# Kernel tuning notes

Measured on AMD Instinct MI355X. Metric: run time of the kernel, lower is better.

## Reference

```python
import jax, jax.numpy as jnp
import numpy as np

B, N, C, H = 2, 4096, 384, 6
HD = C // H          # 64
HALF = C // 2        # 192 = 3 pose heads * HD
MLP_H = 4 * C        # 1536
EPS = 1e-5


def _ln(x, g, b):
    m = jnp.mean(x, axis=-1, keepdims=True)
    v = jnp.mean((x - m) ** 2, axis=-1, keepdims=True)
    return (x - m) * jax.lax.rsqrt(v + EPS) * g + b


def setup_inputs() -> dict:
    key = jax.random.key(0)
    ks = jax.random.split(key, 6)
    s = 0.02
    return {
        "x": jax.random.normal(ks[0], (B, N, C), dtype=jnp.float32),
        "qkv_w": jax.random.normal(ks[1], (3 * C, C), dtype=jnp.float32) * s,
        "proj_w": jax.random.normal(ks[2], (C, HALF), dtype=jnp.float32) * s,
        "proj_b": jnp.zeros((C,), jnp.float32),
        "gamma1": jnp.ones((C,), jnp.float32),
        "beta1": jnp.zeros((C,), jnp.float32),
        "gamma2": jnp.ones((C,), jnp.float32),
        "beta2": jnp.zeros((C,), jnp.float32),
        "fc1_w": jax.random.normal(ks[3], (MLP_H, C), dtype=jnp.float32) * s,
        "fc1_b": jnp.zeros((MLP_H,), jnp.float32),
        "fc2_w": jax.random.normal(ks[4], (C, MLP_H), dtype=jnp.float32) * s,
        "fc2_b": jnp.zeros((C,), jnp.float32),
    }


def reference(x, qkv_w, proj_w, proj_b, gamma1, beta1, gamma2, beta2,
              fc1_w, fc1_b, fc2_w, fc2_b):
    b, n, c = x.shape
    scale = HD ** -0.5
    # --- attention on pre-norm input ---
    h = _ln(x, gamma1, beta1)
    qkv = (h @ qkv_w.T).reshape(b, n, 3, H, HD).transpose(2, 0, 3, 1, 4)  # [3,B,H,N,HD]
    q, k, v = qkv[0], qkv[1], qkv[2]
    # obj heads 0:3 -> sigmoid attention; pose heads 3:6 -> softmax attention
    attn_obj = jax.nn.sigmoid(jnp.einsum('bhnd,bhmd->bhnm', q[:, :3], k[:, :3]) * scale)
    attn_pose = jax.nn.softmax(jnp.einsum('bhnd,bhmd->bhnm', q[:, 3:], k[:, 3:]) * scale, axis=-1)
    # chained combine: pose-attn applied after obj-attn on pose values
    ctx = jnp.einsum('bhnm,bhmd->bhnd', attn_obj, v[:, 3:])      # [B,3,N,HD]
    ctx = jnp.einsum('bhnm,bhmd->bhnd', attn_pose, ctx)          # [B,3,N,HD]
    ctx = ctx.transpose(0, 2, 1, 3).reshape(b, n, HALF)          # [B,N,C/2]
    x = x + (ctx @ proj_w.T + proj_b)
    # --- MLP ---
    h2 = _ln(x, gamma2, beta2)
    mlp = jax.nn.gelu(h2 @ fc1_w.T + fc1_b, approximate=False) @ fc2_w.T + fc2_b
    return (x + mlp, attn_obj)
```

## Files before the change

### kernel.cpp

```cpp
#include <hip/hip_runtime.h>
#include <hip/hip_bf16.h>
#include <cmath>


typedef __hip_bfloat16 bf16;
typedef __attribute__((ext_vector_type(8))) short short8;
typedef __attribute__((ext_vector_type(4))) short s16x4;
typedef __attribute__((ext_vector_type(4))) float f32x4;

#define MFMA16(a, b, c) __builtin_amdgcn_mfma_f32_16x16x32_bf16((a), (b), (c), 0, 0, 0)

__device__ __forceinline__ void async16(const void* g, void* l) {
  __builtin_amdgcn_global_load_lds(
      (const __attribute__((address_space(1))) void*)g,
      (__attribute__((address_space(3))) void*)l, 16, 0, 0);
}

__device__ __forceinline__ short f2bs(float v) {
  union { bf16 b; short s; } u;
  u.b = __float2bfloat16(v);
  return u.s;
}

__global__ void cvt_f32_bf16(const float* __restrict__ in, bf16* __restrict__ out, int n) {
  int i = blockIdx.x * 256 + threadIdx.x;
  if (i < n) out[i] = __float2bfloat16(in[i]);
}

__global__ __launch_bounds__(128) void ln_fwd(const float* __restrict__ x,
                                              const float* __restrict__ gamma,
                                              const float* __restrict__ beta,
                                              bf16* __restrict__ out) {
  const int row = blockIdx.x;
  const int t = threadIdx.x;
  const float* xr = x + (size_t)row * 384;
  float v0 = xr[t], v1 = xr[t + 128], v2 = xr[t + 256];
  float s = v0 + v1 + v2;
  float q = v0 * v0 + v1 * v1 + v2 * v2;
#pragma unroll
  for (int m = 1; m < 64; m <<= 1) {
    s += __shfl_xor(s, m);
    q += __shfl_xor(q, m);
  }
  __shared__ float ss[2], qq[2];
  int w = t >> 6;
  if ((t & 63) == 0) { ss[w] = s; qq[w] = q; }
  __syncthreads();
  s = ss[0] + ss[1];
  q = qq[0] + qq[1];
  float mean = s * (1.0f / 384.0f);
  float var = q * (1.0f / 384.0f) - mean * mean;
  float rstd = rsqrtf(var + 1e-5f);
  bf16* orow = out + (size_t)row * 384;
  orow[t]       = __float2bfloat16((v0 - mean) * rstd * gamma[t]       + beta[t]);
  orow[t + 128] = __float2bfloat16((v1 - mean) * rstd * gamma[t + 128] + beta[t + 128]);
  orow[t + 256] = __float2bfloat16((v2 - mean) * rstd * gamma[t + 256] + beta[t + 256]);
}

template <int EPI>
__global__ __launch_bounds__(256) void gemm_nt(const bf16* __restrict__ A,
                                               const bf16* __restrict__ Bm, int M, int N, int K,
                                               const float* __restrict__ bias,
                                               const float* __restrict__ resid,
                                               float* __restrict__ outf,
                                               bf16* __restrict__ outb) {
  __shared__ __attribute__((aligned(16))) short As[2][64][64];
  __shared__ __attribute__((aligned(16))) short Bs[2][128][64];
  const int t = threadIdx.x;
  const int l = t & 63;
  const int w = t >> 6;
  const int bm = blockIdx.y * 64, bn = blockIdx.x * 128;
  const int r8 = t >> 3, c8 = (t & 7) * 8;

  const bf16* Ab = A + (size_t)(bm + r8) * K + c8;
  const bf16* Bb = Bm + (size_t)(bn + r8) * K + c8;

  f32x4 acc[4][2] = {};

  auto stage = [&](int kt, int bf) {
    async16(Ab + kt, &As[bf][r8][c8]);
    async16(Ab + (size_t)32 * K + kt, &As[bf][32 + r8][c8]);
#pragma unroll
    for (int i = 0; i < 4; ++i)
      async16(Bb + (size_t)(i * 32) * K + kt, &Bs[bf][i * 32 + r8][c8]);
  };

  stage(0, 0);
  int bf = 0;
  for (int kt = 0; kt < K; kt += 64) {
    __syncthreads();
    if (kt + 64 < K) stage(kt + 64, bf ^ 1);
#pragma unroll
    for (int ks = 0; ks < 2; ++ks) {
      short8 a[4], b[2];
#pragma unroll
      for (int i = 0; i < 4; ++i)
        a[i] = *(const short8*)&As[bf][i * 16 + (l & 15)][ks * 32 + (l >> 4) * 8];
#pragma unroll
      for (int j = 0; j < 2; ++j)
        b[j] = *(const short8*)&Bs[bf][w * 32 + j * 16 + (l & 15)][ks * 32 + (l >> 4) * 8];
#pragma unroll
      for (int i = 0; i < 4; ++i)
#pragma unroll
        for (int j = 0; j < 2; ++j) acc[i][j] = MFMA16(a[i], b[j], acc[i][j]);
    }
    bf ^= 1;
  }

#pragma unroll
  for (int i = 0; i < 4; ++i) {
#pragma unroll
    for (int j = 0; j < 2; ++j) {
#pragma unroll
      for (int r = 0; r < 4; ++r) {
        int row = bm + i * 16 + (l >> 4) * 4 + r;
        int col = bn + w * 32 + j * 16 + (l & 15);
        float v = acc[i][j][r];
        if (EPI == 0) {
          int three = col / 384;
          int rem = col - three * 384;
          int head = rem >> 6;
          int hd = rem & 63;
          int bb = row >> 12;
          int n = row & 4095;
          const size_t QSZ = (size_t)2 * 6 * 4096 * 64;
          if (three < 2) {
            size_t di = ((((size_t)three * 2 + bb) * 6 + head) * 4096 + n) * 64 + hd;
            outb[di] = __float2bfloat16(v);
          } else {
            size_t di = 2 * QSZ + (((size_t)bb * 6 + head) * 64 + hd) * 4096 + n;
            outb[di] = __float2bfloat16(v);
          }
        } else if (EPI == 1 || EPI == 3) {
          size_t di = (size_t)row * N + col;
          outf[di] = v + bias[col] + resid[di];
        } else if (EPI == 2) {
          float u = v + bias[col];
          float z = 0.7978845608f * (u + 0.044715f * u * u * u);
          float e = __builtin_amdgcn_exp2f(z * 2.885390082f);
          float th = 1.0f - 2.0f * __builtin_amdgcn_rcpf(e + 1.0f);
          outb[(size_t)row * N + col] = __float2bfloat16(0.5f * u * (1.0f + th));
        }
      }
    }
  }
}

template <int MODE>
__global__ __launch_bounds__(256) void attn_fused(const bf16* __restrict__ qkvb,
                                                  const bf16* __restrict__ vsrc_base,
                                                  float* __restrict__ aout,
                                                  float* __restrict__ part,
                                                  float* __restrict__ lpart) {
  const int bh = blockIdx.z, b = bh / 3, h = bh - b * 3;
  const int row0 = blockIdx.x * 64;
  const int cbase = blockIdx.y * 1024;
  const int t = threadIdx.x, l = t & 63, w = t >> 6;

  const size_t HSZ = (size_t)4096 * 64;
  const size_t QSZ = (size_t)2 * 6 * 4096 * 64;
  const int head = (MODE == 0) ? h : h + 3;
  const bf16* qp = qkvb + (size_t)(b * 6 + head) * HSZ;
  const bf16* kp = qkvb + QSZ + (size_t)(b * 6 + head) * HSZ;
  const bf16* vbase = (MODE == 0)
      ? qkvb + 2 * QSZ + (size_t)((b * 6 + h + 3) * 64) * 4096
      : vsrc_base + (size_t)(bh * 64) * 4096;

  __shared__ __attribute__((aligned(16))) short Ks[2][64][64];
  __shared__ __attribute__((aligned(16))) short Vs[2][64][64];
  __shared__ __attribute__((aligned(16))) float Sf[4][16][68];

  short8 aq[2];
  {
    int qrow = row0 + w * 16 + (l & 15);
    const bf16* qq = qp + (size_t)qrow * 64 + (l >> 4) * 8;
    aq[0] = *(const short8*)(qq);
    aq[1] = *(const short8*)(qq + 32);
  }

  const int r8 = t >> 3, c8 = (t & 7) * 8;
  const int sc = c8 ^ ((r8 & 7) * 8);

  auto stage = [&](int ct, int bf) {
    const bf16* kb = kp + (size_t)(cbase + ct * 64) * 64;
    async16(kb + (size_t)r8 * 64 + sc, &Ks[bf][r8][c8]);
    async16(kb + (size_t)(32 + r8) * 64 + sc, &Ks[bf][32 + r8][c8]);
    const bf16* vb = vbase + cbase + ct * 64;
    async16(vb + (size_t)r8 * 4096 + sc, &Vs[bf][r8][c8]);
    async16(vb + (size_t)(32 + r8) * 4096 + sc, &Vs[bf][32 + r8][c8]);
  };

  f32x4 cacc[4] = {};
  float lp[4] = {0.f, 0.f, 0.f, 0.f};
  const float K1 = -0.18033688f;
  const float K2 = 0.18033688f;

  float* sfw = &Sf[w][0][0];
  stage(0, 0);
  int bf = 0;
  for (int ct = 0; ct < 16; ++ct) {
    __syncthreads();
    if (ct < 15) stage(ct + 1, bf ^ 1);

    f32x4 sacc[4] = {};
#pragma unroll
    for (int ks = 0; ks < 2; ++ks) {
#pragma unroll
      for (int j = 0; j < 4; ++j) {
        int rr = j * 16 + (l & 15);
        int ec = (ks * 32 + (l >> 4) * 8) ^ ((rr & 7) * 8);
        short8 bk = *(const short8*)&Ks[bf][rr][ec];
        sacc[j] = MFMA16(aq[ks], bk, sacc[j]);
      }
    }

#pragma unroll
    for (int j = 0; j < 4; ++j) {
#pragma unroll
      for (int r = 0; r < 4; ++r) {
        float s = sacc[j][r];
        float v;
        if (MODE == 0) {
          v = __builtin_amdgcn_rcpf(1.0f + __builtin_amdgcn_exp2f(s * K1));
        } else {
          v = __builtin_amdgcn_exp2f(s * K2);
          lp[r] += v;
        }
        sfw[((l >> 4) * 4 + r) * 68 + j * 16 + (l & 15)] = v;
      }
    }

    short8 pa[2];
#pragma unroll
    for (int ks = 0; ks < 2; ++ks) {
      const float* sp = &sfw[(l & 15) * 68 + ks * 32 + (l >> 4) * 8];
      f32x4 f0 = *(const f32x4*)sp;
      f32x4 f1 = *(const f32x4*)(sp + 4);
      short8 a;
#pragma unroll
      for (int e = 0; e < 4; ++e) a[e] = f2bs(f0[e]);
#pragma unroll
      for (int e = 0; e < 4; ++e) a[4 + e] = f2bs(f1[e]);
      pa[ks] = a;
    }

    if (MODE == 0) {
      float* ab = aout + (size_t)bh * 4096 * 4096 +
                  (size_t)(row0 + w * 16) * 4096 + cbase + ct * 64;
#pragma unroll
      for (int i = 0; i < 4; ++i) {
        f32x4 vv = *(const f32x4*)&sfw[(4 * i + (l >> 4)) * 68 + (l & 15) * 4];
        *(f32x4*)(ab + (size_t)(4 * i + (l >> 4)) * 4096 + (l & 15) * 4) = vv;
      }
    }

#pragma unroll
    for (int ks = 0; ks < 2; ++ks) {
#pragma unroll
      for (int j = 0; j < 4; ++j) {
        int rr = j * 16 + (l & 15);
        int ec = (ks * 32 + (l >> 4) * 8) ^ ((rr & 7) * 8);
        short8 bv = *(const short8*)&Vs[bf][rr][ec];
        cacc[j] = MFMA16(pa[ks], bv, cacc[j]);
      }
    }
    bf ^= 1;
  }

  float* pb = part + ((size_t)(blockIdx.y * 6 + bh) * 4096 + row0 + w * 16) * 64;
#pragma unroll
  for (int j = 0; j < 4; ++j)
#pragma unroll
    for (int r = 0; r < 4; ++r)
      pb[(size_t)((l >> 4) * 4 + r) * 64 + j * 16 + (l & 15)] = cacc[j][r];

  if (MODE == 1) {
#pragma unroll
    for (int r = 0; r < 4; ++r) {
#pragma unroll
      for (int m = 1; m < 16; m <<= 1) lp[r] += __shfl_xor(lp[r], m);
    }
    if ((l & 15) == 0) {
      float* lb = lpart + (size_t)(blockIdx.y * 6 + bh) * 4096 + row0 + w * 16 + (l >> 4) * 4;
#pragma unroll
      for (int r = 0; r < 4; ++r) lb[r] = lp[r];
    }
  }
}

__global__ __launch_bounds__(256) void reduce_obj(const float* __restrict__ part,
                                                  bf16* __restrict__ ctx1T) {
  const int bh = blockIdx.y, n0 = blockIdx.x * 64, t = threadIdx.x;
  __shared__ short S[64][66];
  const int nr = t >> 2, h0 = (t & 3) * 16;
  const size_t CS = (size_t)6 * 4096 * 64;
  const float* p0 = part + ((size_t)bh * 4096 + n0 + nr) * 64 + h0;
#pragma unroll
  for (int q = 0; q < 4; ++q) {
    f32x4 s = {};
#pragma unroll
    for (int c = 0; c < 4; ++c) s += *(const f32x4*)(p0 + c * CS + q * 4);
#pragma unroll
    for (int e = 0; e < 4; ++e) S[nr][h0 + q * 4 + e] = f2bs(s[e]);
  }
  __syncthreads();
  const int hd = t >> 2, nb = (t & 3) * 16;
  short8 o0, o1;
#pragma unroll
  for (int k = 0; k < 8; ++k) o0[k] = S[nb + k][hd];
#pragma unroll
  for (int k = 0; k < 8; ++k) o1[k] = S[nb + 8 + k][hd];
  short* dst = (short*)(ctx1T + ((size_t)bh * 64 + hd) * 4096 + n0 + nb);
  *(short8*)dst = o0;
  *(short8*)(dst + 8) = o1;
}

__global__ __launch_bounds__(256) void reduce_pose(const float* __restrict__ part,
                                                   const float* __restrict__ lpart,
                                                   bf16* __restrict__ ctxf) {
  const int idx = blockIdx.x * 256 + threadIdx.x;
  const int hd4 = idx & 15;
  const int n = (idx >> 4) & 4095;
  const int bh = idx >> 16;
  const size_t CS = (size_t)6 * 4096 * 64, CL = (size_t)6 * 4096;
  f32x4 s = {};
  float lt = 0.f;
#pragma unroll
  for (int c = 0; c < 4; ++c) {
    s += *(const f32x4*)(part + c * CS + ((size_t)bh * 4096 + n) * 64 + hd4 * 4);
    lt += lpart[c * CL + (size_t)bh * 4096 + n];
  }
  float inv = 1.0f / lt;
  int b = bh / 3, h = bh - b * 3;
  s16x4 o;
#pragma unroll
  for (int e = 0; e < 4; ++e) o[e] = f2bs(s[e] * inv);
  *(s16x4*)(ctxf + ((size_t)b * 4096 + n) * 192 + h * 64 + hd4 * 4) = o;
}

extern "C" void kernel_launch(void* const* d_in, const int* in_sizes, int n_in,
                              void* d_out, int out_size, void* d_ws, size_t ws_size,
                              hipStream_t stream) {
  const float* x      = (const float*)d_in[0];
  const float* qkv_w  = (const float*)d_in[1];
  const float* proj_w = (const float*)d_in[2];
  const float* proj_b = (const float*)d_in[3];
  const float* gamma1 = (const float*)d_in[4];
  const float* beta1  = (const float*)d_in[5];
  const float* gamma2 = (const float*)d_in[6];
  const float* beta2  = (const float*)d_in[7];
  const float* fc1_w  = (const float*)d_in[8];
  const float* fc1_b  = (const float*)d_in[9];
  const float* fc2_w  = (const float*)d_in[10];
  const float* fc2_b  = (const float*)d_in[11];

  float* out_x = (float*)d_out;
  float* out_attn = out_x + (size_t)2 * 4096 * 384;

  char* ws = (char*)d_ws;
  size_t off = 0;
  auto alloc = [&](size_t bytes) -> void* {
    void* p = ws + off;
    off += (bytes + 255) & ~(size_t)255;
    return p;
  };
  bf16* qkv_w_b  = (bf16*)alloc((size_t)1152 * 384 * 2);
  bf16* proj_w_b = (bf16*)alloc((size_t)384 * 192 * 2);
  bf16* fc1_w_b  = (bf16*)alloc((size_t)1536 * 384 * 2);
  bf16* fc2_w_b  = (bf16*)alloc((size_t)384 * 1536 * 2);
  bf16* h1    = (bf16*)alloc((size_t)8192 * 384 * 2);
  bf16* qkvb  = (bf16*)alloc((size_t)3 * 2 * 6 * 4096 * 64 * 2);
  float* c1p  = (float*)alloc((size_t)4 * 6 * 4096 * 64 * 4);
  float* cpp  = (float*)alloc((size_t)4 * 6 * 4096 * 64 * 4);
  float* lpp  = (float*)alloc((size_t)4 * 6 * 4096 * 4);
  bf16* ctx1T = (bf16*)alloc((size_t)6 * 64 * 4096 * 2);
  bf16* ctxf  = (bf16*)alloc((size_t)2 * 4096 * 192 * 2);
  float* x2   = (float*)alloc((size_t)8192 * 384 * 4);
  bf16* h2    = (bf16*)alloc((size_t)8192 * 384 * 2);
  bf16* h3    = (bf16*)alloc((size_t)8192 * 1536 * 2);

  cvt_f32_bf16<<<(1152 * 384 + 255) / 256, 256, 0, stream>>>(qkv_w, qkv_w_b, 1152 * 384);
  cvt_f32_bf16<<<(384 * 192 + 255) / 256, 256, 0, stream>>>(proj_w, proj_w_b, 384 * 192);
  cvt_f32_bf16<<<(1536 * 384 + 255) / 256, 256, 0, stream>>>(fc1_w, fc1_w_b, 1536 * 384);
  cvt_f32_bf16<<<(384 * 1536 + 255) / 256, 256, 0, stream>>>(fc2_w, fc2_w_b, 384 * 1536);

  ln_fwd<<<8192, 128, 0, stream>>>(x, gamma1, beta1, h1);

  gemm_nt<0><<<dim3(9, 128), 256, 0, stream>>>(h1, qkv_w_b, 8192, 1152, 384,
                                               nullptr, nullptr, nullptr, qkvb);

  attn_fused<0><<<dim3(64, 4, 6), 256, 0, stream>>>(qkvb, nullptr, out_attn, c1p, nullptr);
  reduce_obj<<<dim3(64, 6), 256, 0, stream>>>(c1p, ctx1T);
  attn_fused<1><<<dim3(64, 4, 6), 256, 0, stream>>>(qkvb, ctx1T, nullptr, cpp, lpp);
  reduce_pose<<<1536, 256, 0, stream>>>(cpp, lpp, ctxf);

  gemm_nt<1><<<dim3(3, 128), 256, 0, stream>>>(ctxf, proj_w_b, 8192, 384, 192,
                                               proj_b, x, x2, nullptr);
  ln_fwd<<<8192, 128, 0, stream>>>(x2, gamma2, beta2, h2);
  gemm_nt<2><<<dim3(12, 128), 256, 0, stream>>>(h2, fc1_w_b, 8192, 1536, 384,
                                                fc1_b, nullptr, nullptr, h3);
  gemm_nt<3><<<dim3(3, 128), 256, 0, stream>>>(h3, fc2_w_b, 8192, 384, 1536,
                                               fc2_b, x2, out_x, nullptr);
}
```

Before: 310.8 us.

## Enlarge GEMM and attention tiles, merge weight casts, one-wave-per-row LayerNorm

Attention blocks now process 128 query rows instead of 64, so each staged K/V tile is reused across two row fragments and half as many blocks reload K/V. The QKV and fc1 GEMMs move to a 128x128 tile with a 2x2 wave layout but lose double buffering, since staging is now synchronous with two barriers per K step. The four weight-cast launches become one kernel, and LayerNorm uses one wave per row with no shared-memory reduction. The single-buffered GEMM exposes global-load latency, and the larger attention tile adds register pressure and halves the grid.

```diff
diff --git a/kernel.cpp b/kernel.cpp
--- a/kernel.cpp
+++ b/kernel.cpp
@@ -22,99 +22,102 @@
   return u.s;
 }
 
-__global__ void cvt_f32_bf16(const float* __restrict__ in, bf16* __restrict__ out, int n) {
+__global__ void cvt_all(const float* __restrict__ a, const float* __restrict__ b,
+                        const float* __restrict__ c, const float* __restrict__ d,
+                        bf16* __restrict__ oa, bf16* __restrict__ ob,
+                        bf16* __restrict__ oc, bf16* __restrict__ od) {
   int i = blockIdx.x * 256 + threadIdx.x;
-  if (i < n) out[i] = __float2bfloat16(in[i]);
-}
-
-__global__ __launch_bounds__(128) void ln_fwd(const float* __restrict__ x,
+  const int n0 = 1152 * 384, n1 = 384 * 192, n2 = 1536 * 384, n3 = 384 * 1536;
+  if (i < n0) { oa[i] = __float2bfloat16(a[i]); return; }
+  i -= n0;
+  if (i < n1) { ob[i] = __float2bfloat16(b[i]); return; }
+  i -= n1;
+  if (i < n2) { oc[i] = __float2bfloat16(c[i]); return; }
+  i -= n2;
+  if (i < n3) { od[i] = __float2bfloat16(d[i]); }
+}
+
+__global__ __launch_bounds__(256) void ln_fwd(const float* __restrict__ x,
                                               const float* __restrict__ gamma,
                                               const float* __restrict__ beta,
                                               bf16* __restrict__ out) {
-  const int row = blockIdx.x;
-  const int t = threadIdx.x;
+  const int row = blockIdx.x * 4 + (threadIdx.x >> 6);
+  const int l = threadIdx.x & 63;
   const float* xr = x + (size_t)row * 384;
-  float v0 = xr[t], v1 = xr[t + 128], v2 = xr[t + 256];
-  float s = v0 + v1 + v2;
-  float q = v0 * v0 + v1 * v1 + v2 * v2;
+  float v[6];
+  float s = 0.f, q = 0.f;
+#pragma unroll
+  for (int i = 0; i < 6; ++i) {
+    v[i] = xr[l + i * 64];
+    s += v[i];
+    q += v[i] * v[i];
+  }
 #pragma unroll
   for (int m = 1; m < 64; m <<= 1) {
     s += __shfl_xor(s, m);
     q += __shfl_xor(q, m);
   }
-  __shared__ float ss[2], qq[2];
-  int w = t >> 6;
-  if ((t & 63) == 0) { ss[w] = s; qq[w] = q; }
-  __syncthreads();
-  s = ss[0] + ss[1];
-  q = qq[0] + qq[1];
   float mean = s * (1.0f / 384.0f);
   float var = q * (1.0f / 384.0f) - mean * mean;
   float rstd = rsqrtf(var + 1e-5f);
   bf16* orow = out + (size_t)row * 384;
-  orow[t]       = __float2bfloat16((v0 - mean) * rstd * gamma[t]       + beta[t]);
-  orow[t + 128] = __float2bfloat16((v1 - mean) * rstd * gamma[t + 128] + beta[t + 128]);
-  orow[t + 256] = __float2bfloat16((v2 - mean) * rstd * gamma[t + 256] + beta[t + 256]);
+#pragma unroll
+  for (int i = 0; i < 6; ++i)
+    orow[l + i * 64] = __float2bfloat16((v[i] - mean) * rstd * gamma[l + i * 64] + beta[l + i * 64]);
 }
 
 template <int EPI>
-__global__ __launch_bounds__(256) void gemm_nt(const bf16* __restrict__ A,
+__global__ __launch_bounds__(256) void gemm128(const bf16* __restrict__ A,
                                                const bf16* __restrict__ Bm, int M, int N, int K,
                                                const float* __restrict__ bias,
-                                               const float* __restrict__ resid,
-                                               float* __restrict__ outf,
                                                bf16* __restrict__ outb) {
-  __shared__ __attribute__((aligned(16))) short As[2][64][64];
-  __shared__ __attribute__((aligned(16))) short Bs[2][128][64];
+  __shared__ __attribute__((aligned(16))) short As[128][64];
+  __shared__ __attribute__((aligned(16))) short Bs[128][64];
   const int t = threadIdx.x;
   const int l = t & 63;
   const int w = t >> 6;
-  const int bm = blockIdx.y * 64, bn = blockIdx.x * 128;
-  const int r8 = t >> 3, c8 = (t & 7) * 8;
-
+  const int wm = w >> 1, wn = w & 1;
+  const int bm = blockIdx.y * 128, bn = blockIdx.x * 128;
+
+  f32x4 acc[4][4] = {};
+  const int r8 = t >> 3;
+  const int c8 = (t & 7) * 8;
   const bf16* Ab = A + (size_t)(bm + r8) * K + c8;
   const bf16* Bb = Bm + (size_t)(bn + r8) * K + c8;
 
-  f32x4 acc[4][2] = {};
-
-  auto stage = [&](int kt, int bf) {
-    async16(Ab + kt, &As[bf][r8][c8]);
-    async16(Ab + (size_t)32 * K + kt, &As[bf][32 + r8][c8]);
-#pragma unroll
-    for (int i = 0; i < 4; ++i)
-      async16(Bb + (size_t)(i * 32) * K + kt, &Bs[bf][i * 32 + r8][c8]);
-  };
-
-  stage(0, 0);
-  int bf = 0;
   for (int kt = 0; kt < K; kt += 64) {
     __syncthreads();
-    if (kt + 64 < K) stage(kt + 64, bf ^ 1);
+#pragma unroll
+    for (int i = 0; i < 4; ++i)
+      async16(Ab + (size_t)(i * 32) * K + kt, &As[i * 32 + r8][c8]);
+#pragma unroll
+    for (int i = 0; i < 4; ++i)
+      async16(Bb + (size_t)(i * 32) * K + kt, &Bs[i * 32 + r8][c8]);
+    __syncthreads();
 #pragma unroll
     for (int ks = 0; ks < 2; ++ks) {
-      short8 a[4], b[2];
+      short8 a[4], b[4];
 #pragma unroll
       for (int i = 0; i < 4; ++i)
-        a[i] = *(const short8*)&As[bf][i * 16 + (l & 15)][ks * 32 + (l >> 4) * 8];
-#pragma unroll
-      for (int j = 0; j < 2; ++j)
-        b[j] = *(const short8*)&Bs[bf][w * 32 + j * 16 + (l & 15)][ks * 32 + (l >> 4) * 8];
+        a[i] = *(const short8*)&As[wm * 64 + i * 16 + (l & 15)][ks * 32 + (l >> 4) * 8];
 #pragma unroll
       for (int i = 0; i < 4; ++i)
-#pragma unroll
-        for (int j = 0; j < 2; ++j) acc[i][j] = MFMA16(a[i], b[j], acc[i][j]);
-    }
-    bf ^= 1;
+        b[i] = *(const short8*)&Bs[wn * 64 + i * 16 + (l & 15)][ks * 32 + (l >> 4) * 8];
+#pragma unroll
+      for (int i = 0; i < 4; ++i)
+#pragma unroll
+        for (int j = 0; j < 4; ++j) acc[i][j] = MFMA16(a[i], b[j], acc[i][j]);
+    }
   }
 
 #pragma unroll
   for (int i = 0; i < 4; ++i) {
 #pragma unroll
-    for (int j = 0; j < 2; ++j) {
+    for (int j = 0; j < 4; ++j) {
 #pragma unroll
       for (int r = 0; r < 4; ++r) {
-        int row = bm + i * 16 + (l >> 4) * 4 + r;
-        int col = bn + w * 32 + j * 16 + (l & 15);
+        int row = bm + wm * 64 + i * 16 + (l >> 4) * 4 + r;
+        int col = bn + wn * 64 + j * 16 + (l & 15);
         float v = acc[i][j][r];
         if (EPI == 0) {
           int three = col / 384;
@@ -131,16 +134,76 @@
             size_t di = 2 * QSZ + (((size_t)bb * 6 + head) * 64 + hd) * 4096 + n;
             outb[di] = __float2bfloat16(v);
           }
-        } else if (EPI == 1 || EPI == 3) {
-          size_t di = (size_t)row * N + col;
-          outf[di] = v + bias[col] + resid[di];
-        } else if (EPI == 2) {
+        } else {
           float u = v + bias[col];
           float z = 0.7978845608f * (u + 0.044715f * u * u * u);
           float e = __builtin_amdgcn_exp2f(z * 2.885390082f);
           float th = 1.0f - 2.0f * __builtin_amdgcn_rcpf(e + 1.0f);
           outb[(size_t)row * N + col] = __float2bfloat16(0.5f * u * (1.0f + th));
         }
+      }
+    }
+  }
+}
+
+__global__ __launch_bounds__(256) void gemm64(const bf16* __restrict__ A,
+                                              const bf16* __restrict__ Bm, int M, int N, int K,
+                                              const float* __restrict__ bias,
+                                              const float* __restrict__ resid,
+                                              float* __restrict__ outf) {
+  __shared__ __attribute__((aligned(16))) short As[2][64][64];
+  __shared__ __attribute__((aligned(16))) short Bs[2][128][64];
+  const int t = threadIdx.x;
+  const int l = t & 63;
+  const int w = t >> 6;
+  const int bm = blockIdx.y * 64, bn = blockIdx.x * 128;
+  const int r8 = t >> 3, c8 = (t & 7) * 8;
+
+  const bf16* Ab = A + (size_t)(bm + r8) * K + c8;
+  const bf16* Bb = Bm + (size_t)(bn + r8) * K + c8;
+
+  f32x4 acc[4][2] = {};
+
+  auto stage = [&](int kt, int bf) {
+    async16(Ab + kt, &As[bf][r8][c8]);
+    async16(Ab + (size_t)32 * K + kt, &As[bf][32 + r8][c8]);
+#pragma unroll
+    for (int i = 0; i < 4; ++i)
+      async16(Bb + (size_t)(i * 32) * K + kt, &Bs[bf][i * 32 + r8][c8]);
+  };
+
+  stage(0, 0);
+  int bf = 0;
+  for (int kt = 0; kt < K; kt += 64) {
+    __syncthreads();
+    if (kt + 64 < K) stage(kt + 64, bf ^ 1);
+#pragma unroll
+    for (int ks = 0; ks < 2; ++ks) {
+      short8 a[4], b[2];
+#pragma unroll
+      for (int i = 0; i < 4; ++i)
+        a[i] = *(const short8*)&As[bf][i * 16 + (l & 15)][ks * 32 + (l >> 4) * 8];
+#pragma unroll
+      for (int j = 0; j < 2; ++j)
+        b[j] = *(const short8*)&Bs[bf][w * 32 + j * 16 + (l & 15)][ks * 32 + (l >> 4) * 8];
+#pragma unroll
+      for (int i = 0; i < 4; ++i)
+#pragma unroll
+        for (int j = 0; j < 2; ++j) acc[i][j] = MFMA16(a[i], b[j], acc[i][j]);
+    }
+    bf ^= 1;
+  }
+
+#pragma unroll
+  for (int i = 0; i < 4; ++i) {
+#pragma unroll
+    for (int j = 0; j < 2; ++j) {
+#pragma unroll
+      for (int r = 0; r < 4; ++r) {
+        int row = bm + i * 16 + (l >> 4) * 4 + r;
+        int col = bn + w * 32 + j * 16 + (l & 15);
+        size_t di = (size_t)row * N + col;
+        outf[di] = acc[i][j][r] + bias[col] + resid[di];
       }
     }
   }
@@ -153,7 +216,7 @@
                                                   float* __restrict__ part,
                                                   float* __restrict__ lpart) {
   const int bh = blockIdx.z, b = bh / 3, h = bh - b * 3;
-  const int row0 = blockIdx.x * 64;
+  const int row0 = blockIdx.x * 128;
   const int cbase = blockIdx.y * 1024;
   const int t = threadIdx.x, l = t & 63, w = t >> 6;
 
@@ -170,12 +233,13 @@
   __shared__ __attribute__((aligned(16))) short Vs[2][64][64];
   __shared__ __attribute__((aligned(16))) float Sf[4][16][68];
 
-  short8 aq[2];
-  {
-    int qrow = row0 + w * 16 + (l & 15);
+  short8 aq[2][2];
+#pragma unroll
+  for (int rf = 0; rf < 2; ++rf) {
+    int qrow = row0 + rf * 64 + w * 16 + (l & 15);
     const bf16* qq = qp + (size_t)qrow * 64 + (l >> 4) * 8;
-    aq[0] = *(const short8*)(qq);
-    aq[1] = *(const short8*)(qq + 32);
+    aq[rf][0] = *(const short8*)(qq);
+    aq[rf][1] = *(const short8*)(qq + 32);
   }
 
   const int r8 = t >> 3, c8 = (t & 7) * 8;
@@ -190,8 +254,8 @@
     async16(vb + (size_t)(32 + r8) * 4096 + sc, &Vs[bf][32 + r8][c8]);
   };
 
-  f32x4 cacc[4] = {};
-  float lp[4] = {0.f, 0.f, 0.f, 0.f};
+  f32x4 cacc[2][4] = {};
+  float lp[2][4] = {};
   const float K1 = -0.18033688f;
   const float K2 = 0.18033688f;
 
@@ -202,88 +266,97 @@
     __syncthreads();
     if (ct < 15) stage(ct + 1, bf ^ 1);
 
-    f32x4 sacc[4] = {};
-#pragma unroll
-    for (int ks = 0; ks < 2; ++ks) {
+#pragma unroll
+    for (int rf = 0; rf < 2; ++rf) {
+      f32x4 sacc[4] = {};
+#pragma unroll
+      for (int ks = 0; ks < 2; ++ks) {
+#pragma unroll
+        for (int j = 0; j < 4; ++j) {
+          int rr = j * 16 + (l & 15);
+          int ec = (ks * 32 + (l >> 4) * 8) ^ ((rr & 7) * 8);
+          short8 bk = *(const short8*)&Ks[bf][rr][ec];
+          sacc[j] = MFMA16(aq[rf][ks], bk, sacc[j]);
+        }
+      }
+
 #pragma unroll
       for (int j = 0; j < 4; ++j) {
-        int rr = j * 16 + (l & 15);
-        int ec = (ks * 32 + (l >> 4) * 8) ^ ((rr & 7) * 8);
-        short8 bk = *(const short8*)&Ks[bf][rr][ec];
-        sacc[j] = MFMA16(aq[ks], bk, sacc[j]);
-      }
-    }
-
-#pragma unroll
-    for (int j = 0; j < 4; ++j) {
+#pragma unroll
+        for (int r = 0; r < 4; ++r) {
+          float s = sacc[j][r];
+          float v;
+          if (MODE == 0) {
+            v = __builtin_amdgcn_rcpf(1.0f + __builtin_amdgcn_exp2f(s * K1));
+          } else {
+            v = __builtin_amdgcn_exp2f(s * K2);
+            lp[rf][r] += v;
+          }
+          sfw[((l >> 4) * 4 + r) * 68 + j * 16 + (l & 15)] = v;
+        }
+      }
+
+      short8 pa[2];
+#pragma unroll
+      for (int ks = 0; ks < 2; ++ks) {
+        const float* sp = &sfw[(l & 15) * 68 + ks * 32 + (l >> 4) * 8];
+        f32x4 f0 = *(const f32x4*)sp;
+        f32x4 f1 = *(const f32x4*)(sp + 4);
+        short8 a;
+#pragma unroll
+        for (int e = 0; e < 4; ++e) a[e] = f2bs(f0[e]);
+#pragma unroll
+        for (int e = 0; e < 4; ++e) a[4 + e] = f2bs(f1[e]);
+        pa[ks] = a;
+      }
+
+      if (MODE == 0) {
+        float* ab = aout + (size_t)bh * 4096 * 4096 +
+                    (size_t)(row0 + rf * 64 + w * 16) * 4096 + cbase + ct * 64;
+#pragma unroll
+        for (int i = 0; i < 4; ++i) {
+          f32x4 vv = *(const f32x4*)&sfw[(4 * i + (l >> 4)) * 68 + (l & 15) * 4];
+          *(f32x4*)(ab + (size_t)(4 * i + (l >> 4)) * 4096 + (l & 15) * 4) = vv;
+        }
+      }
+
+#pragma unroll
+      for (int ks = 0; ks < 2; ++ks) {
+#pragma unroll
+        for (int j = 0; j < 4; ++j) {
+          int rr = j * 16 + (l & 15);
+          int ec = (ks * 32 + (l >> 4) * 8) ^ ((rr & 7) * 8);
+          short8 bv = *(const short8*)&Vs[bf][rr][ec];
+          cacc[rf][j] = MFMA16(pa[ks], bv, cacc[rf][j]);
+        }
+      }
+    }
+    bf ^= 1;
+  }
+
+#pragma unroll
+  for (int rf = 0; rf < 2; ++rf) {
+    float* pb = part + ((size_t)(blockIdx.y * 6 + bh) * 4096 + row0 + rf * 64 + w * 16) * 64;
+#pragma unroll
+    for (int j = 0; j < 4; ++j)
+#pragma unroll
+      for (int r = 0; r < 4; ++r)
+        pb[(size_t)((l >> 4) * 4 + r) * 64 + j * 16 + (l & 15)] = cacc[rf][j][r];
+  }
+
+  if (MODE == 1) {
+#pragma unroll
+    for (int rf = 0; rf < 2; ++rf) {
 #pragma unroll
       for (int r = 0; r < 4; ++r) {
-        float s = sacc[j][r];
-        float v;
-        if (MODE == 0) {
-          v = __builtin_amdgcn_rcpf(1.0f + __builtin_amdgcn_exp2f(s * K1));
-        } else {
-          v = __builtin_amdgcn_exp2f(s * K2);
-          lp[r] += v;
-        }
-        sfw[((l >> 4) * 4 + r) * 68 + j * 16 + (l & 15)] = v;
-      }
-    }
-
-    short8 pa[2];
-#pragma unroll
-    for (int ks = 0; ks < 2; ++ks) {
-      const float* sp = &sfw[(l & 15) * 68 + ks * 32 + (l >> 4) * 8];
-      f32x4 f0 = *(const f32x4*)sp;
-      f32x4 f1 = *(const f32x4*)(sp + 4);
-      short8 a;
-#pragma unroll
-      for (int e = 0; e < 4; ++e) a[e] = f2bs(f0[e]);
-#pragma unroll
-      for (int e = 0; e < 4; ++e) a[4 + e] = f2bs(f1[e]);
-      pa[ks] = a;
-    }
-
-    if (MODE == 0) {
-      float* ab = aout + (size_t)bh * 4096 * 4096 +
-                  (size_t)(row0 + w * 16) * 4096 + cbase + ct * 64;
-#pragma unroll
-      for (int i = 0; i < 4; ++i) {
-        f32x4 vv = *(const f32x4*)&sfw[(4 * i + (l >> 4)) * 68 + (l & 15) * 4];
-        *(f32x4*)(ab + (size_t)(4 * i + (l >> 4)) * 4096 + (l & 15) * 4) = vv;
-      }
-    }
-
-#pragma unroll
-    for (int ks = 0; ks < 2; ++ks) {
-#pragma unroll
-      for (int j = 0; j < 4; ++j) {
-        int rr = j * 16 + (l & 15);
-        int ec = (ks * 32 + (l >> 4) * 8) ^ ((rr & 7) * 8);
-        short8 bv = *(const short8*)&Vs[bf][rr][ec];
-        cacc[j] = MFMA16(pa[ks], bv, cacc[j]);
-      }
-    }
-    bf ^= 1;
-  }
-
-  float* pb = part + ((size_t)(blockIdx.y * 6 + bh) * 4096 + row0 + w * 16) * 64;
-#pragma unroll
-  for (int j = 0; j < 4; ++j)
-#pragma unroll
-    for (int r = 0; r < 4; ++r)
-      pb[(size_t)((l >> 4) * 4 + r) * 64 + j * 16 + (l & 15)] = cacc[j][r];
-
-  if (MODE == 1) {
-#pragma unroll
-    for (int r = 0; r < 4; ++r) {
-#pragma unroll
-      for (int m = 1; m < 16; m <<= 1) lp[r] += __shfl_xor(lp[r], m);
-    }
-    if ((l & 15) == 0) {
-      float* lb = lpart + (size_t)(blockIdx.y * 6 + bh) * 4096 + row0 + w * 16 + (l >> 4) * 4;
-#pragma unroll
-      for (int r = 0; r < 4; ++r) lb[r] = lp[r];
+#pragma unroll
+        for (int m = 1; m < 16; m <<= 1) lp[rf][r] += __shfl_xor(lp[rf][r], m);
+      }
+      if ((l & 15) == 0) {
+        float* lb = lpart + (size_t)(blockIdx.y * 6 + bh) * 4096 + row0 + rf * 64 + w * 16 + (l >> 4) * 4;
+#pragma unroll
+        for (int r = 0; r < 4; ++r) lb[r] = lp[rf][r];
+      }
     }
   }
 }
@@ -379,26 +452,24 @@
   bf16* h2    = (bf16*)alloc((size_t)8192 * 384 * 2);
   bf16* h3    = (bf16*)alloc((size_t)8192 * 1536 * 2);
 
-  cvt_f32_bf16<<<(1152 * 384 + 255) / 256, 256, 0, stream>>>(qkv_w, qkv_w_b, 1152 * 384);
-  cvt_f32_bf16<<<(384 * 192 + 255) / 256, 256, 0, stream>>>(proj_w, proj_w_b, 384 * 192);
-  cvt_f32_bf16<<<(1536 * 384 + 255) / 256, 256, 0, stream>>>(fc1_w, fc1_w_b, 1536 * 384);
-  cvt_f32_bf16<<<(384 * 1536 + 255) / 256, 256, 0, stream>>>(fc2_w, fc2_w_b, 384 * 1536);
-
-  ln_fwd<<<8192, 128, 0, stream>>>(x, gamma1, beta1, h1);
-
-  gemm_nt<0><<<dim3(9, 128), 256, 0, stream>>>(h1, qkv_w_b, 8192, 1152, 384,
-                                               nullptr, nullptr, nullptr, qkvb);
-
-  attn_fused<0><<<dim3(64, 4, 6), 256, 0, stream>>>(qkvb, nullptr, out_attn, c1p, nullptr);
+  cvt_all<<<6624, 256, 0, stream>>>(qkv_w, proj_w, fc1_w, fc2_w,
+                                    qkv_w_b, proj_w_b, fc1_w_b, fc2_w_b);
+
+  ln_fwd<<<2048, 256, 0, stream>>>(x, gamma1, beta1, h1);
+
+  gemm128<0><<<dim3(9, 64), 256, 0, stream>>>(h1, qkv_w_b, 8192, 1152, 384,
+                                              nullptr, qkvb);
+
+  attn_fused<0><<<dim3(32, 4, 6), 256, 0, stream>>>(qkvb, nullptr, out_attn, c1p, nullptr);
   reduce_obj<<<dim3(64, 6), 256, 0, stream>>>(c1p, ctx1T);
-  attn_fused<1><<<dim3(64, 4, 6), 256, 0, stream>>>(qkvb, ctx1T, nullptr, cpp, lpp);
+  attn_fused<1><<<dim3(32, 4, 6), 256, 0, stream>>>(qkvb, ctx1T, nullptr, cpp, lpp);
   reduce_pose<<<1536, 256, 0, stream>>>(cpp, lpp, ctxf);
 
-  gemm_nt<1><<<dim3(3, 128), 256, 0, stream>>>(ctxf, proj_w_b, 8192, 384, 192,
-                                               proj_b, x, x2, nullptr);
-  ln_fwd<<<8192, 128, 0, stream>>>(x2, gamma2, beta2, h2);
-  gemm_nt<2><<<dim3(12, 128), 256, 0, stream>>>(h2, fc1_w_b, 8192, 1536, 384,
-                                                fc1_b, nullptr, nullptr, h3);
-  gemm_nt<3><<<dim3(3, 128), 256, 0, stream>>>(h3, fc2_w_b, 8192, 384, 1536,
-                                               fc2_b, x2, out_x, nullptr);
-}
+  gemm64<<<dim3(3, 128), 256, 0, stream>>>(ctxf, proj_w_b, 8192, 384, 192,
+                                           proj_b, x, x2);
+  ln_fwd<<<2048, 256, 0, stream>>>(x2, gamma2, beta2, h2);
+  gemm128<2><<<dim3(12, 64), 256, 0, stream>>>(h2, fc1_w_b, 8192, 1536, 384,
+                                               fc1_b, h3);
+  gemm64<<<dim3(3, 128), 256, 0, stream>>>(h3, fc2_w_b, 8192, 384, 1536,
+                                           fc2_b, x2, out_x);
+}
```

Result: no change. 311.5 us (+0.2%).
